# Optimization experiments

Measured on AMD Instinct MI355X. Metric: run time of the kernel, lower is better.

The kernel has to match this reference:

```python
import jax, jax.numpy as jnp
import numpy as np

B, S, D, H = 4, 2048, 1024, 16
HD = D // H  # head_dim = 64


def setup_inputs() -> dict:
    key = jax.random.key(0)
    k1, k2, k3 = jax.random.split(key, 3)
    scale = 0.02
    return {
        "hidden_states": jax.random.normal(k1, (B, S, D), dtype=jnp.float32),
        "W_attn": jax.random.normal(k2, (D, 3 * D), dtype=jnp.float32) * scale,
        "b_attn": jnp.zeros((3 * D,), dtype=jnp.float32),
        "W_proj": jax.random.normal(k3, (D, D), dtype=jnp.float32) * scale,
        "b_proj": jnp.zeros((D,), dtype=jnp.float32),
    }


def reference(hidden_states, W_attn, b_attn, W_proj, b_proj):
    b, s, d = hidden_states.shape
    qkv = hidden_states @ W_attn + b_attn  # [B,S,3D]
    q, k, v = jnp.split(qkv, 3, axis=-1)
    # [B,S,D] -> [B,H,S,hd]
    def to_heads(x):
        return x.reshape(b, s, H, HD).transpose(0, 2, 1, 3)
    q, k, v = to_heads(q), to_heads(k), to_heads(v)
    scores = jnp.einsum("bhqd,bhkd->bhqk", q, k) / jnp.sqrt(jnp.float32(HD))
    causal = jnp.tril(jnp.ones((s, s), dtype=bool))  # [S,S]
    scores = jnp.where(causal[None, None], scores, jnp.float32(-jnp.inf))
    probs = jax.nn.softmax(scores, axis=-1)  # dropout p=0 -> identity (eval)
    out = jnp.einsum("bhqk,bhkd->bhqd", probs, v)  # [B,H,S,hd]
    out = out.transpose(0, 2, 1, 3).reshape(b, s, d)
    return out @ W_proj + b_proj
```

## Files before the change

### kernel.cpp

```cpp
#include <hip/hip_runtime.h>
#include <hip/hip_bf16.h>


typedef float f32x4 __attribute__((ext_vector_type(4)));
typedef __bf16 bf16x8 __attribute__((ext_vector_type(8)));
typedef unsigned short u16x8 __attribute__((ext_vector_type(8)));
typedef unsigned short u16x4 __attribute__((ext_vector_type(4)));

static constexpr int Sq = 2048, Dm = 1024, HD = 64, N3 = 3072;
static constexpr int Mrows = 4 * Sq;
static constexpr float SM_SCALE = 0.18033688011112042f;
static constexpr float SM_BIAS  = -11.541560327111707f;

__device__ __forceinline__ float bf2f(unsigned short u) {
  union { unsigned u32; float f; } x; x.u32 = ((unsigned)u) << 16; return x.f;
}
__device__ __forceinline__ unsigned short f2bf(float f) {
  return __builtin_bit_cast(unsigned short, (__bf16)f);
}
__device__ __forceinline__ f32x4 mfma16(u16x8 a, u16x8 b, f32x4 c) {
  return __builtin_amdgcn_mfma_f32_16x16x32_bf16(
      __builtin_bit_cast(bf16x8, a), __builtin_bit_cast(bf16x8, b), c, 0, 0, 0);
}

__global__ __launch_bounds__(256) void cvt_k(
    const float* __restrict__ in, unsigned short* __restrict__ out, int n) {
  int stride = gridDim.x * 256 * 4;
  for (int i = (blockIdx.x * 256 + threadIdx.x) * 4; i < n; i += stride) {
    f32x4 v = *reinterpret_cast<const f32x4*>(&in[i]);
    u16x4 o;
    #pragma unroll
    for (int j = 0; j < 4; j++) o[j] = f2bf(v[j]);
    *reinterpret_cast<u16x4*>(&out[i]) = o;
  }
}

__global__ __launch_bounds__(256) void tcvt_k(
    const float* __restrict__ in, unsigned short* __restrict__ out,
    int R, int C) {
  __shared__ float tile[32][33];
  int c0 = blockIdx.x * 32, r0 = blockIdx.y * 32;
  int tx = threadIdx.x & 31, ty = threadIdx.x >> 5;
  #pragma unroll
  for (int i = 0; i < 32; i += 8)
    tile[ty + i][tx] = in[(size_t)(r0 + ty + i) * C + c0 + tx];
  __syncthreads();
  #pragma unroll
  for (int i = 0; i < 32; i += 8)
    out[(size_t)(c0 + ty + i) * R + r0 + tx] = f2bf(tile[tx][ty + i]);
}

template <bool OUT_F32>
__global__ __launch_bounds__(256) void gemm_bt(
    const unsigned short* __restrict__ A, const unsigned short* __restrict__ Bt,
    const float* __restrict__ bias, void* __restrict__ Cout,
    int Md, int Nd, int Kd) {
  __shared__ unsigned short Asm[128 * 32];
  __shared__ unsigned short Bsm[128 * 32];
  int t = threadIdx.x;
  int wave = t >> 6, lane = t & 63;
  int lrow = lane & 15, lq = lane >> 4;
  int wr = wave >> 1, wc = wave & 1;
  int bm = blockIdx.y * 128, bn = blockIdx.x * 128;
  f32x4 acc[4][4] = {};

  for (int k0 = 0; k0 < Kd; k0 += 32) {
    __syncthreads();
    #pragma unroll
    for (int c = 0; c < 2; c++) {
      int e = c * 2048 + t * 8;
      int row = e >> 5, col = e & 31;
      const unsigned short* ga = A + (size_t)(bm + row) * Kd + k0 + col;
      const unsigned short* gb = Bt + (size_t)(bn + row) * Kd + k0 + col;
      __builtin_amdgcn_global_load_lds(
          (const __attribute__((address_space(1))) void*)ga,
          (__attribute__((address_space(3))) void*)((char*)Asm + c * 4096 + wave * 1024),
          16, 0, 0);
      __builtin_amdgcn_global_load_lds(
          (const __attribute__((address_space(1))) void*)gb,
          (__attribute__((address_space(3))) void*)((char*)Bsm + c * 4096 + wave * 1024),
          16, 0, 0);
    }
    __syncthreads();

    u16x8 af[4], bfr[4];
    #pragma unroll
    for (int m = 0; m < 4; m++)
      af[m] = *reinterpret_cast<const u16x8*>(&Asm[(wr * 64 + m * 16 + lrow) * 32 + lq * 8]);
    #pragma unroll
    for (int n = 0; n < 4; n++)
      bfr[n] = *reinterpret_cast<const u16x8*>(&Bsm[(wc * 64 + n * 16 + lrow) * 32 + lq * 8]);
    #pragma unroll
    for (int m = 0; m < 4; m++)
      #pragma unroll
      for (int n = 0; n < 4; n++)
        acc[m][n] = mfma16(af[m], bfr[n], acc[m][n]);
  }

  #pragma unroll
  for (int n = 0; n < 4; n++) {
    int col = bn + wc * 64 + n * 16 + lrow;
    float bv = bias[col];
    #pragma unroll
    for (int m = 0; m < 4; m++) {
      #pragma unroll
      for (int j = 0; j < 4; j++) {
        int row = bm + wr * 64 + m * 16 + lq * 4 + j;
        if constexpr (OUT_F32)
          ((float*)Cout)[(size_t)row * Nd + col] = acc[m][n][j] + bv;
        else
          ((unsigned short*)Cout)[(size_t)row * Nd + col] = f2bf(acc[m][n][j] + bv);
      }
    }
  }
}

__global__ __launch_bounds__(512, 4) void attn_k(
    const unsigned short* __restrict__ qkv,
    unsigned short* __restrict__ ao) {
  int bh = blockIdx.y;
  int b = bh >> 4, h = bh & 15;
  int t = threadIdx.x, wave = t >> 6, lane = t & 63;
  int lrow = lane & 15, lq = lane >> 4;

  __shared__ unsigned short Kl[2][64][72];
  __shared__ unsigned short Vt[2][64][72];
  __shared__ unsigned short Pl[8][16][72];

  const size_t base = (size_t)b * Sq * N3;
  const unsigned short* Kbase = qkv + base + Dm + h * HD;
  const unsigned short* Vbase = qkv + base + 2 * Dm + h * HD;

  bool stageK = wave < 4;
  int irow = t >> 2, icol = (t & 3) * 16;
  int vd = t & 63, vkb = (t >> 6) & 3;

  u16x8 ones;
  #pragma unroll
  for (int j = 0; j < 8; j++) ones[j] = 0x3F80;

  u16x8 r0, r1;
  auto prefetch = [&](int kv) {
    if (stageK) {
      const unsigned short* kp = Kbase + (size_t)(kv + irow) * N3 + icol;
      r0 = *reinterpret_cast<const u16x8*>(kp);
      r1 = *reinterpret_cast<const u16x8*>(kp + 8);
    } else {
      const unsigned short* vp = Vbase + (size_t)kv * N3 + vd;
      #pragma unroll
      for (int i = 0; i < 8; i++) {
        r0[i] = vp[(size_t)(vkb * 8 + i) * N3];
        r1[i] = vp[(size_t)(32 + vkb * 8 + i) * N3];
      }
    }
  };

  #pragma unroll 1
  for (int pass = 0; pass < 2; ++pass) {
    int qb = pass ? (int)blockIdx.x : 15 - (int)blockIdx.x;
    int q0 = qb * 128;
    int ntiles = 2 * qb + 2;
    int rwm = q0 + wave * 16;

    u16x8 qf0, qf1;
    {
      const unsigned short* qp =
          qkv + base + (size_t)(rwm + lrow) * N3 + h * HD + lq * 8;
      u16x8 a0 = *reinterpret_cast<const u16x8*>(qp);
      u16x8 a1 = *reinterpret_cast<const u16x8*>(qp + 32);
      #pragma unroll
      for (int j = 0; j < 8; j++) {
        qf0[j] = f2bf(SM_SCALE * bf2f(a0[j]));
        qf1[j] = f2bf(SM_SCALE * bf2f(a1[j]));
      }
    }

    f32x4 oacc[4] = {};
    f32x4 dacc = {};

    if (pass == 0) prefetch(0);

    #pragma unroll 1
    for (int kt = 0; kt < ntiles; ++kt) {
      int kv = kt * 64, bsel = kt & 1;
      if (stageK) {
        *reinterpret_cast<u16x8*>(&Kl[bsel][irow][icol]) = r0;
        *reinterpret_cast<u16x8*>(&Kl[bsel][irow][icol + 8]) = r1;
      } else {
        *reinterpret_cast<u16x8*>(&Vt[bsel][vd][vkb * 8]) = r0;
        *reinterpret_cast<u16x8*>(&Vt[bsel][vd][32 + vkb * 8]) = r1;
      }
      if (kt + 1 < ntiles) prefetch(kv + 64);
      else if (pass == 0) prefetch(0);
      __syncthreads();

      u16x8 kf0[4], kf1[4];
      #pragma unroll
      for (int ct = 0; ct < 4; ct++) {
        kf0[ct] = *reinterpret_cast<const u16x8*>(&Kl[bsel][ct * 16 + lrow][lq * 8]);
        kf1[ct] = *reinterpret_cast<const u16x8*>(&Kl[bsel][ct * 16 + lrow][32 + lq * 8]);
      }
      f32x4 sacc[4];
      #pragma unroll
      for (int ct = 0; ct < 4; ct++)
        sacc[ct] = f32x4{SM_BIAS, SM_BIAS, SM_BIAS, SM_BIAS};
      __builtin_amdgcn_s_setprio(1);
      #pragma unroll
      for (int ct = 0; ct < 4; ct++) {
        sacc[ct] = mfma16(kf0[ct], qf0, sacc[ct]);
        sacc[ct] = mfma16(kf1[ct], qf1, sacc[ct]);
      }
      __builtin_amdgcn_s_setprio(0);

      bool need_mask = kv + 63 > rwm;
      int dlim = rwm - kv + lrow;
      #pragma unroll
      for (int ct = 0; ct < 4; ct++) {
        u16x4 o;
        #pragma unroll
        for (int j = 0; j < 4; j++) {
          float e = exp2f(sacc[ct][j]);
          if (need_mask) e = (16 * ct + 4 * lq + j <= dlim) ? e : 0.f;
          o[j] = f2bf(e);
        }
        *reinterpret_cast<u16x4*>(&Pl[wave][lrow][16 * ct + 4 * lq]) = o;
      }

      u16x8 pa0 = *reinterpret_cast<const u16x8*>(&Pl[wave][lrow][lq * 8]);
      u16x8 pa1 = *reinterpret_cast<const u16x8*>(&Pl[wave][lrow][32 + lq * 8]);
      __builtin_amdgcn_s_setprio(1);
      dacc = mfma16(pa0, ones, dacc);
      dacc = mfma16(pa1, ones, dacc);
      #pragma unroll
      for (int ht = 0; ht < 4; ht++) {
        u16x8 vf0 = *reinterpret_cast<const u16x8*>(&Vt[bsel][ht * 16 + lrow][lq * 8]);
        u16x8 vf1 = *reinterpret_cast<const u16x8*>(&Vt[bsel][ht * 16 + lrow][32 + lq * 8]);
        oacc[ht] = mfma16(pa0, vf0, oacc[ht]);
        oacc[ht] = mfma16(pa1, vf1, oacc[ht]);
      }
      __builtin_amdgcn_s_setprio(0);
    }

    float inv[4];
    #pragma unroll
    for (int j = 0; j < 4; j++) inv[j] = __builtin_amdgcn_rcpf(dacc[j]);
    #pragma unroll
    for (int ht = 0; ht < 4; ht++)
      #pragma unroll
      for (int j = 0; j < 4; j++) {
        int rg = rwm + lq * 4 + j;
        float v = oacc[ht][j] * inv[j];
        ao[(size_t)(b * Sq + rg) * Dm + h * HD + ht * 16 + lrow] = f2bf(v);
      }
  }
}

extern "C" void kernel_launch(void* const* d_in, const int* in_sizes, int n_in,
                              void* d_out, int out_size, void* d_ws, size_t ws_size,
                              hipStream_t stream) {
  const float* hs = (const float*)d_in[0];
  const float* Wa = (const float*)d_in[1];
  const float* ba = (const float*)d_in[2];
  const float* Wp = (const float*)d_in[3];
  const float* bp = (const float*)d_in[4];
  float* out = (float*)d_out;

  char* ws = (char*)d_ws;
  unsigned short* QKV = (unsigned short*)ws;
  unsigned short* WaT = (unsigned short*)(ws + 50331648);
  unsigned short* AO  = (unsigned short*)(ws + 50331648);
  unsigned short* WpT = (unsigned short*)ws;
  unsigned short* hsB = (unsigned short*)d_out;

  cvt_k<<<2048, 256, 0, stream>>>(hs, hsB, Mrows * Dm);
  tcvt_k<<<dim3(96, 32), 256, 0, stream>>>(Wa, WaT, 1024, 3072);
  gemm_bt<false><<<dim3(24, 64), 256, 0, stream>>>(hsB, WaT, ba, QKV, Mrows, N3, Dm);
  attn_k<<<dim3(8, 64), 512, 0, stream>>>(QKV, AO);
  tcvt_k<<<dim3(32, 32), 256, 0, stream>>>(Wp, WpT, 1024, 1024);
  gemm_bt<true><<<dim3(8, 64), 256, 0, stream>>>(AO, WpT, bp, out, Mrows, Dm, Dm);
}
```

Before: 208.0 us.

## Pre-transpose V globally and stage K/V via direct global-to-LDS loads with swizzle

Adds a separate kernel that writes V transposed per head into a scratch region of the output buffer. The attention kernel can then load both K and V tiles with contiguous 16-byte global_load_lds transfers straight into LDS, using an XOR swizzle instead of padding. This replaces the strided scalar V gathers and the register round-trip. The smaller LDS footprint also lets the occupancy hint rise from 4 to 6. The cost is one extra launch plus an extra write and read of V.

```diff
diff --git a/kernel.cpp b/kernel.cpp
--- a/kernel.cpp
+++ b/kernel.cpp
@@ -48,6 +48,32 @@
   #pragma unroll
   for (int i = 0; i < 32; i += 8)
     out[(size_t)(c0 + ty + i) * R + r0 + tx] = f2bf(tile[tx][ty + i]);
+}
+
+__global__ __launch_bounds__(256) void vtr_k(
+    const unsigned short* __restrict__ qkv, unsigned short* __restrict__ vt) {
+  __shared__ unsigned short tile[64][72];
+  int bh = blockIdx.y, b = bh >> 4, h = bh & 15;
+  int kv = blockIdx.x * 64;
+  int t = threadIdx.x;
+  int r = t >> 3, c8 = (t & 7) * 8;
+  const unsigned short* src = qkv + (size_t)b * Sq * N3 + 2 * Dm + h * HD;
+  #pragma unroll
+  for (int hh = 0; hh < 2; hh++) {
+    int k = r + hh * 32;
+    *reinterpret_cast<u16x8*>(&tile[k][c8]) =
+        *reinterpret_cast<const u16x8*>(&src[(size_t)(kv + k) * N3 + c8]);
+  }
+  __syncthreads();
+  unsigned short* dst = vt + (size_t)bh * HD * Sq + kv;
+  #pragma unroll
+  for (int hh = 0; hh < 2; hh++) {
+    int d = r + hh * 32;
+    u16x8 o;
+    #pragma unroll
+    for (int i = 0; i < 8; i++) o[i] = tile[c8 + i][d];
+    *reinterpret_cast<u16x8*>(&dst[(size_t)d * Sq + c8]) = o;
+  }
 }
 
 template <bool OUT_F32>
@@ -115,45 +141,46 @@
   }
 }
 
-__global__ __launch_bounds__(512, 4) void attn_k(
+__global__ __launch_bounds__(512, 6) void attn_k(
     const unsigned short* __restrict__ qkv,
+    const unsigned short* __restrict__ vtg,
     unsigned short* __restrict__ ao) {
   int bh = blockIdx.y;
   int b = bh >> 4, h = bh & 15;
   int t = threadIdx.x, wave = t >> 6, lane = t & 63;
   int lrow = lane & 15, lq = lane >> 4;
 
-  __shared__ unsigned short Kl[2][64][72];
-  __shared__ unsigned short Vt[2][64][72];
+  __shared__ unsigned short Kl[2][64][64];
+  __shared__ unsigned short Vl[2][64][64];
   __shared__ unsigned short Pl[8][16][72];
 
   const size_t base = (size_t)b * Sq * N3;
-  const unsigned short* Kbase = qkv + base + Dm + h * HD;
-  const unsigned short* Vbase = qkv + base + 2 * Dm + h * HD;
-
-  bool stageK = wave < 4;
-  int irow = t >> 2, icol = (t & 3) * 16;
-  int vd = t & 63, vkb = (t >> 6) & 3;
+
+  int srow = t >> 3;
+  int scol = ((t & 7) ^ (srow & 7)) * 8;
+  const unsigned short* Ksrc = qkv + base + Dm + h * HD + (size_t)srow * N3 + scol;
+  const unsigned short* Vsrc = vtg + (size_t)bh * HD * Sq + (size_t)srow * Sq + scol;
+
+  int ca = (lq ^ (lrow & 7)) * 8;
+  int cb = ca ^ 32;
 
   u16x8 ones;
   #pragma unroll
   for (int j = 0; j < 8; j++) ones[j] = 0x3F80;
 
-  u16x8 r0, r1;
-  auto prefetch = [&](int kv) {
-    if (stageK) {
-      const unsigned short* kp = Kbase + (size_t)(kv + irow) * N3 + icol;
-      r0 = *reinterpret_cast<const u16x8*>(kp);
-      r1 = *reinterpret_cast<const u16x8*>(kp + 8);
-    } else {
-      const unsigned short* vp = Vbase + (size_t)kv * N3 + vd;
-      #pragma unroll
-      for (int i = 0; i < 8; i++) {
-        r0[i] = vp[(size_t)(vkb * 8 + i) * N3];
-        r1[i] = vp[(size_t)(32 + vkb * 8 + i) * N3];
-      }
-    }
+  auto stage = [&](int kv, int buf) {
+    __builtin_amdgcn_global_load_lds(
+        (const __attribute__((address_space(1))) void*)(Ksrc + (size_t)kv * N3),
+        (__attribute__((address_space(3))) void*)((char*)&Kl[buf][0][0] + wave * 1024),
+        16, 0, 0);
+    __builtin_amdgcn_global_load_lds(
+        (const __attribute__((address_space(1))) void*)(Vsrc + kv),
+        (__attribute__((address_space(3))) void*)((char*)&Vl[buf][0][0] + wave * 1024),
+        16, 0, 0);
   };
+
+  int cur = 0;
+  stage(0, 0);
 
   #pragma unroll 1
   for (int pass = 0; pass < 2; ++pass) {
@@ -178,27 +205,18 @@
     f32x4 oacc[4] = {};
     f32x4 dacc = {};
 
-    if (pass == 0) prefetch(0);
-
     #pragma unroll 1
     for (int kt = 0; kt < ntiles; ++kt) {
-      int kv = kt * 64, bsel = kt & 1;
-      if (stageK) {
-        *reinterpret_cast<u16x8*>(&Kl[bsel][irow][icol]) = r0;
-        *reinterpret_cast<u16x8*>(&Kl[bsel][irow][icol + 8]) = r1;
-      } else {
-        *reinterpret_cast<u16x8*>(&Vt[bsel][vd][vkb * 8]) = r0;
-        *reinterpret_cast<u16x8*>(&Vt[bsel][vd][32 + vkb * 8]) = r1;
-      }
-      if (kt + 1 < ntiles) prefetch(kv + 64);
-      else if (pass == 0) prefetch(0);
+      int kv = kt * 64;
       __syncthreads();
+      int kvn = (kt + 1 < ntiles) ? kv + 64 : (pass == 0 ? 0 : -1);
+      if (kvn >= 0) stage(kvn, cur ^ 1);
 
       u16x8 kf0[4], kf1[4];
       #pragma unroll
       for (int ct = 0; ct < 4; ct++) {
-        kf0[ct] = *reinterpret_cast<const u16x8*>(&Kl[bsel][ct * 16 + lrow][lq * 8]);
-        kf1[ct] = *reinterpret_cast<const u16x8*>(&Kl[bsel][ct * 16 + lrow][32 + lq * 8]);
+        kf0[ct] = *reinterpret_cast<const u16x8*>(&Kl[cur][ct * 16 + lrow][ca]);
+        kf1[ct] = *reinterpret_cast<const u16x8*>(&Kl[cur][ct * 16 + lrow][cb]);
       }
       f32x4 sacc[4];
       #pragma unroll
@@ -233,12 +251,13 @@
       dacc = mfma16(pa1, ones, dacc);
       #pragma unroll
       for (int ht = 0; ht < 4; ht++) {
-        u16x8 vf0 = *reinterpret_cast<const u16x8*>(&Vt[bsel][ht * 16 + lrow][lq * 8]);
-        u16x8 vf1 = *reinterpret_cast<const u16x8*>(&Vt[bsel][ht * 16 + lrow][32 + lq * 8]);
+        u16x8 vf0 = *reinterpret_cast<const u16x8*>(&Vl[cur][ht * 16 + lrow][ca]);
+        u16x8 vf1 = *reinterpret_cast<const u16x8*>(&Vl[cur][ht * 16 + lrow][cb]);
         oacc[ht] = mfma16(pa0, vf0, oacc[ht]);
         oacc[ht] = mfma16(pa1, vf1, oacc[ht]);
       }
       __builtin_amdgcn_s_setprio(0);
+      cur ^= 1;
     }
 
     float inv[4];
@@ -271,11 +290,13 @@
   unsigned short* AO  = (unsigned short*)(ws + 50331648);
   unsigned short* WpT = (unsigned short*)ws;
   unsigned short* hsB = (unsigned short*)d_out;
+  unsigned short* VT  = (unsigned short*)((char*)d_out + 16777216);
 
   cvt_k<<<2048, 256, 0, stream>>>(hs, hsB, Mrows * Dm);
   tcvt_k<<<dim3(96, 32), 256, 0, stream>>>(Wa, WaT, 1024, 3072);
   gemm_bt<false><<<dim3(24, 64), 256, 0, stream>>>(hsB, WaT, ba, QKV, Mrows, N3, Dm);
-  attn_k<<<dim3(8, 64), 512, 0, stream>>>(QKV, AO);
+  vtr_k<<<dim3(32, 64), 256, 0, stream>>>(QKV, VT);
+  attn_k<<<dim3(8, 64), 512, 0, stream>>>(QKV, VT, AO);
   tcvt_k<<<dim3(32, 32), 256, 0, stream>>>(Wp, WpT, 1024, 1024);
   gemm_bt<true><<<dim3(8, 64), 256, 0, stream>>>(AO, WpT, bp, out, Mrows, Dm, Dm);
 }
```

Result: slower. 219.0 us (+5.3%).
